# Optimization experiments

Hardware: AMD Instinct MI355X
Metric: run time of the kernel (lower is better)

Reference implementation:

```python
import jax, jax.numpy as jnp
import numpy as np
import math

B, N = 1, 512
C_S, C_Z = 384, 128
H, D, PQ, PV = 12, 16, 4, 8
W_C = math.sqrt(2.0 / (9.0 * PQ))
W_L = math.sqrt(1.0 / 3.0)
OUT_IN = H * D + H * PV * 3 + H * PV + H * C_Z  # 2112


def setup_inputs() -> dict:
    key = jax.random.key(0)
    ks = jax.random.split(key, 16)
    s = 0.02
    return {
        "single_representation": jax.random.normal(ks[0], (B, N, C_S), jnp.float32),
        "pair_representation": jax.random.normal(ks[1], (B, N, N, C_Z), jnp.float32),
        "rotations": jax.random.normal(ks[2], (B, N, 3, 3), jnp.float32),
        "translation": jax.random.normal(ks[3], (B, N, 3), jnp.float32),
        "w_q": jax.random.normal(ks[4], (C_S, H * D), jnp.float32) * s,
        "w_k": jax.random.normal(ks[5], (C_S, H * D), jnp.float32) * s,
        "w_v": jax.random.normal(ks[6], (C_S, H * D), jnp.float32) * s,
        "w_qf": jax.random.normal(ks[7], (C_S, 3 * H * PQ), jnp.float32) * s,
        "w_kf": jax.random.normal(ks[8], (C_S, 3 * H * PQ), jnp.float32) * s,
        "w_vf": jax.random.normal(ks[9], (C_S, 3 * H * PV), jnp.float32) * s,
        "w_bias": jax.random.normal(ks[10], (C_Z, H), jnp.float32) * s,
        "head_weights": jnp.zeros((H,), jnp.float32),
        "w_out": jax.random.normal(ks[11], (OUT_IN, C_S), jnp.float32) * s,
        "b_out": jnp.zeros((C_S,), jnp.float32),
    }


def reference(single_representation, pair_representation, rotations, translation,
              w_q, w_k, w_v, w_qf, w_kf, w_vf, w_bias, head_weights, w_out, b_out):
    s = single_representation
    z = pair_representation
    b, n, _ = s.shape

    # scalar q/k/v  [b, n, H, D]
    Q = (s @ w_q).reshape(b, n, H, D)
    K = (s @ w_k).reshape(b, n, H, D)
    V = (s @ w_v).reshape(b, n, H, D)

    # point q/k/v in local frames  [b, n, H, P, 3]
    Qf = (s @ w_qf).reshape(b, n, H, PQ, 3)
    Kf = (s @ w_kf).reshape(b, n, H, PQ, 3)
    Vf = (s @ w_vf).reshape(b, n, H, PV, 3)

    bias = z @ w_bias  # [b, n, n, H]

    # lift points to the global frame
    gq = jnp.einsum('biop,bihqp->bihqo', rotations, Qf) + translation[:, :, None, None, :]
    gk = jnp.einsum('biop,bihqp->bihqo', rotations, Kf) + translation[:, :, None, None, :]

    diff = gq[:, :, None] - gk[:, None]            # [b, i, j, H, PQ, 3]
    gamma = jax.nn.softplus(head_weights)          # [H]
    point_scores = (-0.5 * W_C) * gamma[None, None, None, :] * jnp.sum(diff * diff, axis=(-1, -2))

    rep_scores = jnp.einsum('bihd,bjhd->bijh', Q, K) / math.sqrt(D) + bias
    scores = W_L * (rep_scores + point_scores)     # [b, i, j, H]
    attn = jax.nn.softmax(scores, axis=-2)         # softmax over j

    out_pair = jnp.einsum('bijh,bijd->bihd', attn, z)          # [b, n, H, C_Z]
    out_rep = jnp.einsum('bijh,bjhd->bhid', attn, V)           # [b, H, n, D]

    gv = jnp.einsum('biop,bihqp->bihqo', rotations, Vf) + translation[:, :, None, None, :]
    tmp = jnp.einsum('bijh,bjhqo->bhiqo', attn, gv)            # [b, H, n, PV, 3]

    R_inv = jnp.swapaxes(rotations, -1, -2)
    t_inv = -jnp.einsum('bira,bia->bir', R_inv, translation)
    out_vals = jnp.einsum('biop,bhiqp->bhiqo', R_inv, tmp) + t_inv[:, None, :, None, :]

    out_rep = jnp.transpose(out_rep, (0, 2, 1, 3)).reshape(b, n, H * D)
    out_vals = jnp.transpose(out_vals, (0, 2, 1, 3, 4)).reshape(b, n, H * PV * 3)
    out_norms = jnp.sqrt(jnp.sum(out_vals.reshape(b, n, H * PV, 3) ** 2, axis=-1) + 1e-8)
    out_pair = out_pair.reshape(b, n, H * C_Z)

    cat = jnp.concatenate([out_rep, out_vals, out_norms, out_pair], axis=-1)
    return cat @ w_out + b_out
```

## Files before the change

kernel.cpp:

```cpp
#include <hip/hip_runtime.h>
#include <math.h>

#define N    512
#define CS   384
#define CZ   128
#define H    12
#define D    16
#define PQ   4
#define PV   8
#define CAT_W 2112

#define WC 0.23570226039551584f
#define WL 0.5773502691896258f

#define O_Q    0
#define O_K    98304
#define O_V    196608
#define O_QF   294912
#define O_KF   368640
#define O_VF   442368
#define O_GQ   589824
#define O_GK   663552
#define O_GV   737280
#define O_BIAS 884736
#define O_PART O_BIAS
#define O_CAT  4030464

#define KSPLIT 8
#define KCH    264

__global__ __launch_bounds__(256) void k_proj(
    const float* __restrict__ s,
    const float* __restrict__ wq, const float* __restrict__ wk,
    const float* __restrict__ wv, const float* __restrict__ wqf,
    const float* __restrict__ wkf, const float* __restrict__ wvf,
    float* __restrict__ ws) {
  int id = blockIdx.x * 256 + threadIdx.x;
  int i = id / 1152, p = id % 1152;
  const float* w; int col, W; float* dst;
  if (p < 192)      { w = wq;  col = p;     W = 192; dst = ws + O_Q  + i*192 + col; }
  else if (p < 384) { w = wk;  col = p-192; W = 192; dst = ws + O_K  + i*192 + col; }
  else if (p < 576) { w = wv;  col = p-384; W = 192; dst = ws + O_V  + i*192 + col; }
  else if (p < 720) { w = wqf; col = p-576; W = 144; dst = ws + O_QF + i*144 + col; }
  else if (p < 864) { w = wkf; col = p-720; W = 144; dst = ws + O_KF + i*144 + col; }
  else              { w = wvf; col = p-864; W = 288; dst = ws + O_VF + i*288 + col; }
  const float* srow = s + i*CS;
  float acc = 0.f;
  #pragma unroll 8
  for (int k = 0; k < CS; ++k) acc += srow[k] * w[k*W + col];
  *dst = acc;
}

__global__ __launch_bounds__(256) void k_lift(
    const float* __restrict__ rot, const float* __restrict__ trans,
    float* __restrict__ ws) {
  int id = blockIdx.x * 256 + threadIdx.x;
  int i = id / 192, pt = id % 192;
  const float* src; float* dst;
  if (pt < 48)      { src = ws + O_QF + i*144 + pt*3;      dst = ws + O_GQ + i*144 + pt*3; }
  else if (pt < 96) { src = ws + O_KF + i*144 + (pt-48)*3; dst = ws + O_GK + i*144 + (pt-48)*3; }
  else              { src = ws + O_VF + i*288 + (pt-96)*3; dst = ws + O_GV + i*288 + (pt-96)*3; }
  float l0 = src[0], l1 = src[1], l2 = src[2];
  const float* R = rot + i*9;
  const float* T = trans + i*3;
  #pragma unroll
  for (int o = 0; o < 3; ++o)
    dst[o] = R[o*3+0]*l0 + R[o*3+1]*l1 + R[o*3+2]*l2 + T[o];
}

__global__ __launch_bounds__(256) void k_bias(
    const float* __restrict__ z, const float* __restrict__ wb,
    float* __restrict__ ws) {
  __shared__ float wbl[CZ*H];
  int t = threadIdx.x;
  for (int idx = t; idx < CZ*H; idx += 256) wbl[idx] = wb[idx];
  __syncthreads();
  int id = blockIdx.x * 256 + t;
  int i = id / N, j = id % N;
  const float4* zr = (const float4*)(z + (size_t)(i*N + j) * CZ);
  float acc[H];
  #pragma unroll
  for (int h = 0; h < H; ++h) acc[h] = 0.f;
  #pragma unroll 4
  for (int k4 = 0; k4 < CZ/4; ++k4) {
    float4 v = zr[k4];
    int c = k4*4;
    #pragma unroll
    for (int h = 0; h < H; ++h)
      acc[h] += v.x*wbl[(c+0)*H+h] + v.y*wbl[(c+1)*H+h]
              + v.z*wbl[(c+2)*H+h] + v.w*wbl[(c+3)*H+h];
  }
  float* dst = ws + O_BIAS + (size_t)(i*N + j) * H;
  #pragma unroll
  for (int h = 0; h < H; ++h) dst[h] = acc[h];
}

__global__ __launch_bounds__(256) void k_attn(
    const float* __restrict__ z, const float* __restrict__ rot,
    const float* __restrict__ trans, const float* __restrict__ hw,
    float* __restrict__ ws) {
  __shared__ float sc[N*H];
  __shared__ float Qi[H*D];
  __shared__ float gqi[H*PQ*3];
  __shared__ float tmpP[H*PV*3];
  __shared__ float coef[H];
  int i = blockIdx.x;
  int t = threadIdx.x;

  if (t < 192) Qi[t]  = ws[O_Q  + (size_t)i*192 + t];
  if (t < 144) gqi[t] = ws[O_GQ + (size_t)i*144 + t];
  if (t < H) {
    float x = hw[t];
    float sp = fmaxf(x, 0.f) + log1pf(__expf(-fabsf(x)));
    coef[t] = -0.5f * WC * sp;
  }
  __syncthreads();

  const float* Kg   = ws + O_K;
  const float* gk   = ws + O_GK;
  const float* bias = ws + O_BIAS + (size_t)i*N*H;
  for (int task = t; task < N*H; task += 256) {
    int j = task / H, h = task % H;
    const float* Kr = Kg + j*192 + h*16;
    const float* Qr = Qi + h*16;
    float rep = 0.f;
    #pragma unroll
    for (int d = 0; d < 16; ++d) rep += Qr[d] * Kr[d];
    rep = rep * 0.25f + bias[j*H + h];
    const float* gkr = gk + j*144 + h*12;
    const float* gqr = gqi + h*12;
    float pt = 0.f;
    #pragma unroll
    for (int r = 0; r < 12; ++r) { float d = gqr[r] - gkr[r]; pt += d*d; }
    sc[j*H + h] = WL * (rep + coef[h]*pt);
  }
  __syncthreads();

  int wv = t >> 6, lane = t & 63;
  for (int h = wv; h < H; h += 4) {
    float m = -1e30f;
    for (int j = lane; j < N; j += 64) m = fmaxf(m, sc[j*H+h]);
    #pragma unroll
    for (int off = 32; off; off >>= 1) m = fmaxf(m, __shfl_xor(m, off));
    float e = 0.f;
    for (int j = lane; j < N; j += 64) {
      float v = __expf(sc[j*H+h] - m);
      sc[j*H+h] = v; e += v;
    }
    #pragma unroll
    for (int off = 32; off; off >>= 1) e += __shfl_xor(e, off);
    float inv = 1.f / e;
    for (int j = lane; j < N; j += 64) sc[j*H+h] *= inv;
  }
  __syncthreads();

  float* cat = ws + O_CAT + (size_t)i*CAT_W;
  const float* Vg  = ws + O_V;
  const float* gvv = ws + O_GV;
  for (int task = t; task < 480; task += 256) {
    if (task < 192) {
      int h = task >> 4;
      float acc = 0.f;
      #pragma unroll 4
      for (int j = 0; j < N; ++j) acc += sc[j*H+h] * Vg[j*192 + task];
      cat[task] = acc;
    } else {
      int u = task - 192;
      int h = u / 24;
      float acc = 0.f;
      #pragma unroll 4
      for (int j = 0; j < N; ++j) acc += sc[j*H+h] * gvv[j*288 + u];
      tmpP[u] = acc;
    }
  }

  {
    int g = t >> 7, c = t & 127;
    float acc[6];
    #pragma unroll
    for (int k = 0; k < 6; ++k) acc[k] = 0.f;
    const float* zr = z + (size_t)i*N*CZ + c;
    #pragma unroll 4
    for (int j = 0; j < N; ++j) {
      float zv = zr[(size_t)j*CZ];
      #pragma unroll
      for (int k = 0; k < 6; ++k) acc[k] += sc[j*H + (k*2+g)] * zv;
    }
    #pragma unroll
    for (int k = 0; k < 6; ++k) cat[576 + (k*2+g)*128 + c] = acc[k];
  }
  __syncthreads();

  if (t < 96) {
    int h = t >> 3, q = t & 7;
    const float* R = rot + i*9;
    float tp[3];
    #pragma unroll
    for (int p = 0; p < 3; ++p) tp[p] = tmpP[h*24 + q*3 + p] - trans[i*3 + p];
    float nrm = 1e-8f;
    #pragma unroll
    for (int o = 0; o < 3; ++o) {
      float v = R[o]*tp[0] + R[3+o]*tp[1] + R[6+o]*tp[2];
      cat[192 + h*24 + q*3 + o] = v;
      nrm += v*v;
    }
    cat[480 + h*8 + q] = sqrtf(nrm);
  }
}

__global__ __launch_bounds__(128) void k_out_part(
    const float* __restrict__ wo, const float* __restrict__ ws,
    float* __restrict__ part) {
  __shared__ float catT[KCH][16];
  int rt = blockIdx.x, ct = blockIdx.y, kc = blockIdx.z;
  int t = threadIdx.x;
  int i0 = rt * 16;
  int c  = ct * 128 + t;
  int k0 = kc * KCH;
  const float* cat = ws + O_CAT;
  for (int idx = t; idx < 16*KCH; idx += 128) {
    int r = idx / KCH, k = idx % KCH;
    catT[k][r] = cat[(size_t)(i0 + r) * CAT_W + k0 + k];
  }
  __syncthreads();
  float acc[16];
  #pragma unroll
  for (int r = 0; r < 16; ++r) acc[r] = 0.f;
  const float* wp = wo + (size_t)k0 * 384 + c;
  #pragma unroll 4
  for (int k = 0; k < KCH; ++k) {
    float wv = wp[(size_t)k * 384];
    const float* a = catT[k];
    #pragma unroll
    for (int r = 0; r < 16; ++r) acc[r] += a[r] * wv;
  }
  float* dst = part + (size_t)kc * (N*CS) + (size_t)i0 * 384 + c;
  #pragma unroll
  for (int r = 0; r < 16; ++r) dst[(size_t)r * 384] = acc[r];
}

__global__ __launch_bounds__(256) void k_out_red(
    const float* __restrict__ bo, const float* __restrict__ ws,
    float* __restrict__ out) {
  int id = blockIdx.x * 256 + threadIdx.x;
  int c4 = id % 96;
  float4 acc = ((const float4*)bo)[c4];
  const float* part = ws + O_PART;
  #pragma unroll
  for (int s = 0; s < KSPLIT; ++s) {
    float4 p = *(const float4*)(part + (size_t)s * (N*CS) + (size_t)id * 4);
    acc.x += p.x; acc.y += p.y; acc.z += p.z; acc.w += p.w;
  }
  ((float4*)out)[id] = acc;
}

extern "C" void kernel_launch(void* const* d_in, const int* in_sizes, int n_in,
                              void* d_out, int out_size, void* d_ws, size_t ws_size,
                              hipStream_t stream) {
  const float* s     = (const float*)d_in[0];
  const float* z     = (const float*)d_in[1];
  const float* rot   = (const float*)d_in[2];
  const float* trans = (const float*)d_in[3];
  const float* wq    = (const float*)d_in[4];
  const float* wk    = (const float*)d_in[5];
  const float* wv    = (const float*)d_in[6];
  const float* wqf   = (const float*)d_in[7];
  const float* wkf   = (const float*)d_in[8];
  const float* wvf   = (const float*)d_in[9];
  const float* wb    = (const float*)d_in[10];
  const float* hw    = (const float*)d_in[11];
  const float* wo    = (const float*)d_in[12];
  const float* bo    = (const float*)d_in[13];
  float* out = (float*)d_out;
  float* ws  = (float*)d_ws;

  hipLaunchKernelGGL(k_proj, dim3(512*1152/256), dim3(256), 0, stream,
                     s, wq, wk, wv, wqf, wkf, wvf, ws);
  hipLaunchKernelGGL(k_lift, dim3(512*192/256), dim3(256), 0, stream,
                     rot, trans, ws);
  hipLaunchKernelGGL(k_bias, dim3(512*512/256), dim3(256), 0, stream,
                     z, wb, ws);
  hipLaunchKernelGGL(k_attn, dim3(512), dim3(256), 0, stream,
                     z, rot, trans, hw, ws);
  hipLaunchKernelGGL(k_out_part, dim3(32, 3, KSPLIT), dim3(128), 0, stream,
                     wo, ws, ws + O_PART);
  hipLaunchKernelGGL(k_out_red, dim3(192), dim3(256), 0, stream,
                     bo, ws, out);
}
```

Measured before the change: 470.1 us.

## Transpose K/V/point/bias layouts and split attention into score and apply kernels

Stores K, V and the global key and value points transposed (feature-major), and writes bias head-major so per-head rows of scores are contiguous. The attention kernel is split into a score+softmax kernel that keeps scores in registers and writes the probabilities over the bias buffer, and an apply kernel that reloads them into padded shared memory and does float4 dot products. k_bias now uses four threads per row with shuffle reductions for coalesced z reads, and the pair aggregation splits j across thread halves. This adds a kernel launch and a global round-trip for the attention probabilities in exchange for coalesced accesses and more parallelism.

```diff
diff --git a/kernel.cpp b/kernel.cpp
--- a/kernel.cpp
+++ b/kernel.cpp
@@ -14,20 +14,21 @@
 #define WL 0.5773502691896258f
 
 #define O_Q    0
-#define O_K    98304
-#define O_V    196608
+#define O_KT   98304
+#define O_VT   196608
 #define O_QF   294912
 #define O_KF   368640
 #define O_VF   442368
 #define O_GQ   589824
-#define O_GK   663552
-#define O_GV   737280
+#define O_GKT  663552
+#define O_GVT  737280
 #define O_BIAS 884736
 #define O_PART O_BIAS
 #define O_CAT  4030464
 
 #define KSPLIT 8
 #define KCH    264
+#define ALD    516
 
 __global__ __launch_bounds__(256) void k_proj(
     const float* __restrict__ s,
@@ -39,8 +40,8 @@
   int i = id / 1152, p = id % 1152;
   const float* w; int col, W; float* dst;
   if (p < 192)      { w = wq;  col = p;     W = 192; dst = ws + O_Q  + i*192 + col; }
-  else if (p < 384) { w = wk;  col = p-192; W = 192; dst = ws + O_K  + i*192 + col; }
-  else if (p < 576) { w = wv;  col = p-384; W = 192; dst = ws + O_V  + i*192 + col; }
+  else if (p < 384) { w = wk;  col = p-192; W = 192; dst = ws + O_KT + col*512 + i; }
+  else if (p < 576) { w = wv;  col = p-384; W = 192; dst = ws + O_VT + col*512 + i; }
   else if (p < 720) { w = wqf; col = p-576; W = 144; dst = ws + O_QF + i*144 + col; }
   else if (p < 864) { w = wkf; col = p-720; W = 144; dst = ws + O_KF + i*144 + col; }
   else              { w = wvf; col = p-864; W = 288; dst = ws + O_VF + i*288 + col; }
@@ -56,16 +57,30 @@
     float* __restrict__ ws) {
   int id = blockIdx.x * 256 + threadIdx.x;
   int i = id / 192, pt = id % 192;
-  const float* src; float* dst;
-  if (pt < 48)      { src = ws + O_QF + i*144 + pt*3;      dst = ws + O_GQ + i*144 + pt*3; }
-  else if (pt < 96) { src = ws + O_KF + i*144 + (pt-48)*3; dst = ws + O_GK + i*144 + (pt-48)*3; }
-  else              { src = ws + O_VF + i*288 + (pt-96)*3; dst = ws + O_GV + i*288 + (pt-96)*3; }
-  float l0 = src[0], l1 = src[1], l2 = src[2];
   const float* R = rot + i*9;
   const float* T = trans + i*3;
-  #pragma unroll
-  for (int o = 0; o < 3; ++o)
-    dst[o] = R[o*3+0]*l0 + R[o*3+1]*l1 + R[o*3+2]*l2 + T[o];
+  if (pt < 48) {
+    const float* src = ws + O_QF + i*144 + pt*3;
+    float l0 = src[0], l1 = src[1], l2 = src[2];
+    float* dst = ws + O_GQ + i*144 + pt*3;
+    #pragma unroll
+    for (int o = 0; o < 3; ++o)
+      dst[o] = R[o*3+0]*l0 + R[o*3+1]*l1 + R[o*3+2]*l2 + T[o];
+  } else if (pt < 96) {
+    int p3 = pt - 48;
+    const float* src = ws + O_KF + i*144 + p3*3;
+    float l0 = src[0], l1 = src[1], l2 = src[2];
+    #pragma unroll
+    for (int o = 0; o < 3; ++o)
+      ws[O_GKT + (p3*3+o)*512 + i] = R[o*3+0]*l0 + R[o*3+1]*l1 + R[o*3+2]*l2 + T[o];
+  } else {
+    int p3 = pt - 96;
+    const float* src = ws + O_VF + i*288 + p3*3;
+    float l0 = src[0], l1 = src[1], l2 = src[2];
+    #pragma unroll
+    for (int o = 0; o < 3; ++o)
+      ws[O_GVT + (p3*3+o)*512 + i] = R[o*3+0]*l0 + R[o*3+1]*l1 + R[o*3+2]*l2 + T[o];
+  }
 }
 
 __global__ __launch_bounds__(256) void k_bias(
@@ -75,38 +90,42 @@
   int t = threadIdx.x;
   for (int idx = t; idx < CZ*H; idx += 256) wbl[idx] = wb[idx];
   __syncthreads();
-  int id = blockIdx.x * 256 + t;
-  int i = id / N, j = id % N;
-  const float4* zr = (const float4*)(z + (size_t)(i*N + j) * CZ);
+  int row = blockIdx.x * 64 + (t >> 2);
+  int q = t & 3;
+  const float4* zr = (const float4*)(z + (size_t)row * CZ) + q;
   float acc[H];
   #pragma unroll
   for (int h = 0; h < H; ++h) acc[h] = 0.f;
-  #pragma unroll 4
-  for (int k4 = 0; k4 < CZ/4; ++k4) {
-    float4 v = zr[k4];
-    int c = k4*4;
+  #pragma unroll
+  for (int kk = 0; kk < 8; ++kk) {
+    float4 v = zr[kk*4];
+    int c = (q + kk*4) * 4;
     #pragma unroll
     for (int h = 0; h < H; ++h)
       acc[h] += v.x*wbl[(c+0)*H+h] + v.y*wbl[(c+1)*H+h]
               + v.z*wbl[(c+2)*H+h] + v.w*wbl[(c+3)*H+h];
   }
-  float* dst = ws + O_BIAS + (size_t)(i*N + j) * H;
-  #pragma unroll
-  for (int h = 0; h < H; ++h) dst[h] = acc[h];
-}
-
-__global__ __launch_bounds__(256) void k_attn(
-    const float* __restrict__ z, const float* __restrict__ rot,
-    const float* __restrict__ trans, const float* __restrict__ hw,
-    float* __restrict__ ws) {
-  __shared__ float sc[N*H];
-  __shared__ float Qi[H*D];
-  __shared__ float gqi[H*PQ*3];
-  __shared__ float tmpP[H*PV*3];
+  #pragma unroll
+  for (int h = 0; h < H; ++h) {
+    acc[h] += __shfl_xor(acc[h], 1);
+    acc[h] += __shfl_xor(acc[h], 2);
+  }
+  if (q == 0) {
+    int i = row >> 9, j = row & 511;
+    float* bT = ws + O_BIAS + (size_t)i*6144 + j;
+    #pragma unroll
+    for (int h = 0; h < H; ++h) bT[(size_t)h*512] = acc[h];
+  }
+}
+
+__global__ __launch_bounds__(256) void k_score(
+    const float* __restrict__ hw, float* __restrict__ ws) {
+  __shared__ float Qi[192];
+  __shared__ float gqi[144];
   __shared__ float coef[H];
   int i = blockIdx.x;
   int t = threadIdx.x;
-
+  int wave = t >> 6, lane = t & 63;
   if (t < 192) Qi[t]  = ws[O_Q  + (size_t)i*192 + t];
   if (t < 144) gqi[t] = ws[O_GQ + (size_t)i*144 + t];
   if (t < H) {
@@ -115,81 +134,96 @@
     coef[t] = -0.5f * WC * sp;
   }
   __syncthreads();
-
-  const float* Kg   = ws + O_K;
-  const float* gk   = ws + O_GK;
-  const float* bias = ws + O_BIAS + (size_t)i*N*H;
-  for (int task = t; task < N*H; task += 256) {
-    int j = task / H, h = task % H;
-    const float* Kr = Kg + j*192 + h*16;
-    const float* Qr = Qi + h*16;
-    float rep = 0.f;
-    #pragma unroll
-    for (int d = 0; d < 16; ++d) rep += Qr[d] * Kr[d];
-    rep = rep * 0.25f + bias[j*H + h];
-    const float* gkr = gk + j*144 + h*12;
-    const float* gqr = gqi + h*12;
-    float pt = 0.f;
-    #pragma unroll
-    for (int r = 0; r < 12; ++r) { float d = gqr[r] - gkr[r]; pt += d*d; }
-    sc[j*H + h] = WL * (rep + coef[h]*pt);
-  }
-  __syncthreads();
-
-  int wv = t >> 6, lane = t & 63;
-  for (int h = wv; h < H; h += 4) {
-    float m = -1e30f;
-    for (int j = lane; j < N; j += 64) m = fmaxf(m, sc[j*H+h]);
+  float* att = ws + O_BIAS + (size_t)i*6144;
+  const float* Kt  = ws + O_KT;
+  const float* gkT = ws + O_GKT;
+  for (int hh = 0; hh < 3; ++hh) {
+    int h = wave*3 + hh;
+    float sreg[8];
+    float cf = coef[h];
+    #pragma unroll
+    for (int jb = 0; jb < 8; ++jb) {
+      int j = jb*64 + lane;
+      float rep = 0.f;
+      #pragma unroll
+      for (int d = 0; d < 16; ++d) rep += Qi[h*16+d] * Kt[(h*16+d)*512 + j];
+      float pt = 0.f;
+      #pragma unroll
+      for (int r = 0; r < 12; ++r) {
+        float df = gqi[h*12+r] - gkT[(h*12+r)*512 + j];
+        pt += df*df;
+      }
+      sreg[jb] = WL * (rep * 0.25f + att[(size_t)h*512 + j] + cf*pt);
+    }
+    float m = sreg[0];
+    #pragma unroll
+    for (int jb = 1; jb < 8; ++jb) m = fmaxf(m, sreg[jb]);
     #pragma unroll
     for (int off = 32; off; off >>= 1) m = fmaxf(m, __shfl_xor(m, off));
     float e = 0.f;
-    for (int j = lane; j < N; j += 64) {
-      float v = __expf(sc[j*H+h] - m);
-      sc[j*H+h] = v; e += v;
-    }
+    #pragma unroll
+    for (int jb = 0; jb < 8; ++jb) { sreg[jb] = __expf(sreg[jb] - m); e += sreg[jb]; }
     #pragma unroll
     for (int off = 32; off; off >>= 1) e += __shfl_xor(e, off);
     float inv = 1.f / e;
-    for (int j = lane; j < N; j += 64) sc[j*H+h] *= inv;
-  }
+    #pragma unroll
+    for (int jb = 0; jb < 8; ++jb) att[(size_t)h*512 + jb*64 + lane] = sreg[jb] * inv;
+  }
+}
+
+__global__ __launch_bounds__(256) void k_apply(
+    const float* __restrict__ z, const float* __restrict__ rot,
+    const float* __restrict__ trans, float* __restrict__ ws) {
+  __shared__ float aL[H*ALD];
+  __shared__ float pairOdd[H*128];
+  __shared__ float tmpP[H*PV*3];
+  int i = blockIdx.x;
+  int t = threadIdx.x;
+  const float* attn = ws + O_BIAS + (size_t)i*6144;
+  for (int idx = t; idx < 6144; idx += 256)
+    aL[(idx >> 9)*ALD + (idx & 511)] = attn[idx];
   __syncthreads();
-
   float* cat = ws + O_CAT + (size_t)i*CAT_W;
-  const float* Vg  = ws + O_V;
-  const float* gvv = ws + O_GV;
+
   for (int task = t; task < 480; task += 256) {
-    if (task < 192) {
-      int h = task >> 4;
-      float acc = 0.f;
-      #pragma unroll 4
-      for (int j = 0; j < N; ++j) acc += sc[j*H+h] * Vg[j*192 + task];
-      cat[task] = acc;
-    } else {
-      int u = task - 192;
-      int h = u / 24;
-      float acc = 0.f;
-      #pragma unroll 4
-      for (int j = 0; j < N; ++j) acc += sc[j*H+h] * gvv[j*288 + u];
-      tmpP[u] = acc;
-    }
+    int u, h; const float* src;
+    if (task < 192) { u = task;       h = u >> 4; src = ws + O_VT  + (size_t)u*512; }
+    else            { u = task - 192; h = u / 24; src = ws + O_GVT + (size_t)u*512; }
+    const float4* a4 = (const float4*)(aL + h*ALD);
+    const float4* s4 = (const float4*)src;
+    float4 acc4 = {0.f, 0.f, 0.f, 0.f};
+    #pragma unroll 8
+    for (int j4 = 0; j4 < 128; ++j4) {
+      float4 a = a4[j4], v = s4[j4];
+      acc4.x += a.x*v.x; acc4.y += a.y*v.y; acc4.z += a.z*v.z; acc4.w += a.w*v.w;
+    }
+    float acc = (acc4.x + acc4.y) + (acc4.z + acc4.w);
+    if (task < 192) cat[u] = acc; else tmpP[u] = acc;
   }
 
   {
-    int g = t >> 7, c = t & 127;
-    float acc[6];
-    #pragma unroll
-    for (int k = 0; k < 6; ++k) acc[k] = 0.f;
+    int c = t & 127, g = t >> 7;
+    float acc[H];
+    #pragma unroll
+    for (int h = 0; h < H; ++h) acc[h] = 0.f;
     const float* zr = z + (size_t)i*N*CZ + c;
     #pragma unroll 4
-    for (int j = 0; j < N; ++j) {
+    for (int jj = 0; jj < 256; ++jj) {
+      int j = jj*2 + g;
       float zv = zr[(size_t)j*CZ];
       #pragma unroll
-      for (int k = 0; k < 6; ++k) acc[k] += sc[j*H + (k*2+g)] * zv;
-    }
-    #pragma unroll
-    for (int k = 0; k < 6; ++k) cat[576 + (k*2+g)*128 + c] = acc[k];
-  }
-  __syncthreads();
+      for (int h = 0; h < H; ++h) acc[h] += aL[h*ALD + j] * zv;
+    }
+    if (g) {
+      #pragma unroll
+      for (int h = 0; h < H; ++h) pairOdd[h*128 + c] = acc[h];
+    }
+    __syncthreads();
+    if (!g) {
+      #pragma unroll
+      for (int h = 0; h < H; ++h) cat[576 + h*128 + c] = acc[h] + pairOdd[h*128 + c];
+    }
+  }
 
   if (t < 96) {
     int h = t >> 3, q = t & 7;
@@ -278,10 +312,12 @@
                      s, wq, wk, wv, wqf, wkf, wvf, ws);
   hipLaunchKernelGGL(k_lift, dim3(512*192/256), dim3(256), 0, stream,
                      rot, trans, ws);
-  hipLaunchKernelGGL(k_bias, dim3(512*512/256), dim3(256), 0, stream,
+  hipLaunchKernelGGL(k_bias, dim3(512*512/64), dim3(256), 0, stream,
                      z, wb, ws);
-  hipLaunchKernelGGL(k_attn, dim3(512), dim3(256), 0, stream,
-                     z, rot, trans, hw, ws);
+  hipLaunchKernelGGL(k_score, dim3(512), dim3(256), 0, stream,
+                     hw, ws);
+  hipLaunchKernelGGL(k_apply, dim3(512), dim3(256), 0, stream,
+                     z, rot, trans, ws);
   hipLaunchKernelGGL(k_out_part, dim3(32, 3, KSPLIT), dim3(128), 0, stream,
                      wo, ws, ws + O_PART);
   hipLaunchKernelGGL(k_out_red, dim3(192), dim3(256), 0, stream,
```

After: 497.6 us. 5.9% more time.
